# Kernel tuning notes

Hardware: AMD Instinct MI355X
Metric: run time of the kernel (lower is better)

## Reference

```python
import jax, jax.numpy as jnp
import numpy as np
from itertools import combinations_with_replacement

B, T, F, L, POLY_ORDER = 16, 2048, 128, 16, 3


def _hilbert_filter(N):
    # Matches pytorch_hilbert: H[0]=0, H[1:N//2]=2, H[N//2]=0 (even N)
    h = np.zeros(N, dtype=np.float32)
    if N % 2 == 0:
        h[1:N // 2] = 2.0
    else:
        h[1:(N + 1) // 2] = 2.0
    return jnp.asarray(h)


def hilbert(sig, axis=1):
    N = sig.shape[axis]
    Xf = jnp.fft.fft(sig, axis=axis)
    shape = [1] * sig.ndim
    shape[axis] = N
    return jnp.fft.ifft(Xf * _hilbert_filter(N).reshape(shape), axis=axis)


def _combo_indices(latent, poly_order):
    # static index arrays, grouped by degree n
    return [np.array(list(combinations_with_replacement(range(latent), n)), dtype=np.int32)
            for n in range(1, poly_order + 1)]


def compute_library(z, poly_order):
    # z: [B, T, L] -> theta: [B, T, library_dim]
    feats = []
    for combos in _combo_indices(z.shape[-1], poly_order):
        zc = z[..., combos]            # [B, T, ncomb, n]
        feats.append(jnp.prod(zc, axis=-1))  # [B, T, ncomb]
    analytic = hilbert(z, axis=1)
    feats.append(z)
    feats.append(jnp.abs(analytic))    # extract_real_component
    feats.append(jnp.angle(analytic))  # extract_imaginary_component
    return jnp.concatenate(feats, axis=-1)


def setup_inputs() -> dict:
    key = jax.random.key(0)
    ks = jax.random.split(key, 7)
    lib_dim = L + 2 * L + sum(len(c) for c in _combo_indices(L, POLY_ORDER))
    s_enc = 1.0 / np.sqrt(F)
    s_dec = 1.0 / np.sqrt(L)
    s_sin = 1.0 / np.sqrt(lib_dim)
    return {
        "x": jax.random.normal(ks[0], (B, T, F), dtype=jnp.float32),
        "W_enc": jax.random.uniform(ks[1], (L, F), jnp.float32, -s_enc, s_enc),
        "b_enc": jax.random.uniform(ks[2], (L,), jnp.float32, -s_enc, s_enc),
        "W_dec": jax.random.uniform(ks[3], (F, L), jnp.float32, -s_dec, s_dec),
        "b_dec": jax.random.uniform(ks[4], (F,), jnp.float32, -s_dec, s_dec),
        "W_sindy": jax.random.uniform(ks[5], (L, lib_dim), jnp.float32, -s_sin, s_sin),
        "b_sindy": jax.random.uniform(ks[6], (L,), jnp.float32, -s_sin, s_sin),
    }


def reference(x, W_enc, b_enc, W_dec, b_dec, W_sindy, b_sindy):
    z = jnp.einsum('btf,lf->btl', x, W_enc) + b_enc          # encoder
    theta = compute_library(z, POLY_ORDER)                    # [B,T,lib_dim]
    y_hat = jnp.einsum('btd,ld->btl', theta, W_sindy) + b_sindy
    x_hat = jnp.einsum('btl,fl->btf', z, W_dec) + b_dec       # decoder
    # Jacobian of the linear encoder w.r.t. x is the constant weight matrix
    # broadcast per (b, t): identical math to the O((B*T)^2) autograd version.
    jac_z_x = jnp.broadcast_to(W_enc, (x.shape[0], x.shape[1], L, F))
    return (y_hat, x_hat, z, jac_z_x, W_sindy, W_dec)
```

## Files before the change

### kernel.cpp

```cpp
#include <hip/hip_runtime.h>
#include <math.h>

typedef unsigned short u16;
typedef unsigned int   u32;
typedef __attribute__((ext_vector_type(4))) float f32x4;

#define OFF_ZWS   0
#define OFF_AT    524288
#define OFF_PT    1048576
#define OFF_WT    1572864
#define OFF_ZT    1589120
#define OFF_TWC   2113408
#define OFF_TWS   2115456
#define OFF_PART  2117504

#define HEAD_F4   1577952
#define R1_LO     1577952
#define R1_HI     6577952
#define R2_LO     6577952
#define R2_HI     11577952
#define R3_LO     11577952
#define R3_HI     16777216

__device__ __forceinline__ void jac_range(const float* __restrict__ Wenc,
                                          float* __restrict__ out_jac,
                                          int lo, int hi, int idx, int nth)
{
    const float* wsrc = Wenc + (size_t)((lo + idx) & 511) * 4;
    f32x4 w;
    w.x = wsrc[0]; w.y = wsrc[1]; w.z = wsrc[2]; w.w = wsrc[3];
    f32x4* j4 = (f32x4*)out_jac;
    for (int i = lo + idx; i < hi; i += nth)
        __builtin_nontemporal_store(w, j4 + i);
}

__global__ __launch_bounds__(256) void k1_encdec(
    const float* __restrict__ x, const float* __restrict__ Wenc, const float* __restrict__ benc,
    const float* __restrict__ Wdec, const float* __restrict__ bdec,
    const float* __restrict__ Wsin,
    float* __restrict__ out_z, float* __restrict__ out_xhat,
    float* __restrict__ out_Ws, float* __restrict__ out_Wd,
    float* __restrict__ z_ws, float* __restrict__ z_t, float* __restrict__ wt,
    double* __restrict__ twc_g, double* __restrict__ tws_g,
    float* __restrict__ out_jac)
{
    int tid = threadIdx.x;
    int blk = blockIdx.x;

    if (blk >= 2116) {
        jac_range(Wenc, out_jac, R1_LO, R1_HI, (blk - 2116) * 256 + tid, 262144);
        return;
    }
    if (blk >= 2048) {
        int t0 = (blk - 2048) * 256 + tid;
        if (t0 < 16256) {
            float v = Wsin[t0];
            out_Ws[t0] = v;
            int l = t0 / 1016;
            int d = t0 - l * 1016;
            wt[d * 16 + l] = v;
        } else if (t0 < 17280) {
            int k = t0 - 16256;
            double ang = -6.283185307179586476925286766559 * (double)k / 2048.0;
            double s_, c_;
            sincos(ang, &s_, &c_);
            twc_g[k] = c_;
            tws_g[k] = s_;
        }
        if (t0 < 2048) out_Wd[t0] = Wdec[t0];
        return;
    }

    __shared__ float xs[16][128];
    __shared__ float we[16][132];
    __shared__ float wd[128][17];
    __shared__ float zs[16][16];

    {
        const float4* xv = (const float4*)x + (size_t)blk * 512;
        float* dst = &xs[0][0];
        float4 a = xv[tid], b = xv[tid + 256];
        dst[tid*4+0]=a.x; dst[tid*4+1]=a.y; dst[tid*4+2]=a.z; dst[tid*4+3]=a.w;
        dst[(tid+256)*4+0]=b.x; dst[(tid+256)*4+1]=b.y; dst[(tid+256)*4+2]=b.z; dst[(tid+256)*4+3]=b.w;
    }
    {
        const float4* wev = (const float4*)Wenc;
        #pragma unroll
        for (int h = 0; h < 2; ++h) {
            int vi = tid + h * 256;
            float4 v = wev[vi];
            int base = vi * 4, row = base >> 7, col = base & 127;
            we[row][col+0]=v.x; we[row][col+1]=v.y; we[row][col+2]=v.z; we[row][col+3]=v.w;
        }
    }
    {
        const float4* wdv = (const float4*)Wdec;
        #pragma unroll
        for (int h = 0; h < 2; ++h) {
            int vi = tid + h * 256;
            float4 v = wdv[vi];
            int base = vi * 4, row = base >> 4, col = base & 15;
            wd[row][col+0]=v.x; wd[row][col+1]=v.y; wd[row][col+2]=v.z; wd[row][col+3]=v.w;
        }
    }
    __syncthreads();

    {
        int r = tid >> 4, l = tid & 15;
        float s = 0.f;
        #pragma unroll 8
        for (int f = 0; f < 128; ++f) s += xs[r][f] * we[l][f];
        float zv = s + benc[l];
        zs[r][l] = zv;
        int zo = blk * 256 + tid;
        z_ws[zo]  = zv;
        out_z[zo] = zv;
    }
    __syncthreads();

    {
        int l2 = tid >> 4, r2 = tid & 15;
        z_t[l2 * 32768 + blk * 16 + r2] = zs[r2][l2];
    }

    #pragma unroll
    for (int u = 0; u < 8; ++u) {
        int idx = u * 256 + tid;
        int rr = idx >> 7, f = idx & 127;
        float acc = bdec[f];
        #pragma unroll
        for (int ll = 0; ll < 16; ++ll) acc += zs[rr][ll] * wd[f][ll];
        out_xhat[(size_t)blk * 2048 + idx] = acc;
    }
}

__global__ __launch_bounds__(1024) void k2_hilbert(
    const float* __restrict__ z_t, const double* __restrict__ twc_g,
    const double* __restrict__ tws_g, const float* __restrict__ Wenc,
    float* __restrict__ a_t, float* __restrict__ p_t,
    float* __restrict__ out_jac)
{
    __shared__ double2 c[2048];
    __shared__ double2 tw[1024];

    int tid = threadIdx.x;
    if (blockIdx.x >= 256) {
        jac_range(Wenc, out_jac, R2_LO, R2_HI, (blockIdx.x - 256) * 1024 + tid, 524288);
        return;
    }
    int b = blockIdx.x >> 4, l = blockIdx.x & 15;
    const size_t base = (size_t)l * 32768 + (size_t)b * 2048;
    const float* zp = z_t + base;

    {
        double2 t; t.x = twc_g[tid]; t.y = tws_g[tid];
        tw[tid] = t;
    }
    {
        double2 v0; v0.x = (double)zp[tid];        v0.y = 0.0;
        double2 v1; v1.x = (double)zp[tid + 1024]; v1.y = 0.0;
        c[tid] = v0;
        c[tid + 1024] = v1;
    }
    __syncthreads();

    for (int half = 1024; half >= 1; half >>= 1) {
        int step = 1024 / half;
        int j = tid & (half - 1);
        int pos = ((tid - j) << 1) + j;
        double2 u = c[pos], v = c[pos + half];
        double2 w = tw[j * step];
        double2 s, dsc;
        s.x = u.x + v.x;  s.y = u.y + v.y;
        double br = u.x - v.x, bi = u.y - v.y;
        dsc.x = br * w.x - bi * w.y;
        dsc.y = br * w.y + bi * w.x;
        c[pos] = s;
        c[pos + half] = dsc;
        __syncthreads();
    }

    #pragma unroll
    for (int h = 0; h < 2; ++h) {
        int t = tid + h * 1024;
        double sc = (t == 0 || (t & 1)) ? 0.0 : (2.0 / 2048.0);
        double2 v = c[t];
        v.x *= sc; v.y *= sc;
        c[t] = v;
    }
    __syncthreads();

    for (int half = 1; half <= 1024; half <<= 1) {
        int step = 1024 / half;
        int j = tid & (half - 1);
        int pos = ((tid - j) << 1) + j;
        double2 u = c[pos], v = c[pos + half];
        double2 w = tw[j * step];
        double tr = v.x * w.x + v.y * w.y;
        double ti = v.y * w.x - v.x * w.y;
        double2 p0, p1;
        p0.x = u.x + tr; p0.y = u.y + ti;
        p1.x = u.x - tr; p1.y = u.y - ti;
        c[pos] = p0;
        c[pos + half] = p1;
        __syncthreads();
    }

    #pragma unroll
    for (int h = 0; h < 2; ++h) {
        int t = tid + h * 1024;
        double2 v = c[t];
        a_t[base + t] = (float)sqrt(v.x * v.x + v.y * v.y);
        p_t[base + t] = (float)atan2(v.y, v.x);
    }
}

#define EMIT2(EXPR) do {                                                    \
    if ((unsigned)(d - LO) < 127u) {                                        \
        float vv[2];                                                        \
        _Pragma("unroll") for (int p = 0; p < 2; ++p) vv[p] = (EXPR);       \
        int bb = (d - LO) << 4;                                             \
        _Pragma("unroll") for (int l = 0; l < 16; ++l) {                    \
            float w = lw[bb + l];                                           \
            acc[0][l] = fmaf(vv[0], w, acc[0][l]);                          \
            acc[1][l] = fmaf(vv[1], w, acc[1][l]);                          \
        }                                                                   \
    }                                                                       \
    ++d;                                                                    \
} while (0)

__global__ __launch_bounds__(256, 2) void k3_yhat(
    const float* __restrict__ z_ws, const float* __restrict__ a_t,
    const float* __restrict__ p_t, const float* __restrict__ wt,
    const float* __restrict__ Wenc,
    float* __restrict__ part, float* __restrict__ out_jac)
{
    __shared__ float lw[2032];
    int tid = threadIdx.x;
    if (blockIdx.x >= 512) {
        jac_range(Wenc, out_jac, R3_LO, R3_HI, (blockIdx.x - 512) * 256 + tid, 262144);
        return;
    }
    int slice = blockIdx.x >> 6;
    int ptgrp = blockIdx.x & 63;
    int LO = slice * 127;
    int base = ptgrp * 512;

    {
        const float4* src = (const float4*)(wt + LO * 16);
        float4* dst = (float4*)lw;
        for (int i = tid; i < 508; i += 256) dst[i] = src[i];
    }
    __syncthreads();

    float z[2][16], av[2][16], pv[2][16], acc[2][16];
    #pragma unroll
    for (int p = 0; p < 2; ++p) {
        int bt = base + p * 256 + tid;
        const float4* zp = (const float4*)(z_ws + (size_t)bt * 16);
        #pragma unroll
        for (int q = 0; q < 4; ++q) {
            float4 v = zp[q];
            z[p][q*4+0]=v.x; z[p][q*4+1]=v.y; z[p][q*4+2]=v.z; z[p][q*4+3]=v.w;
        }
    }
    if (LO >= 880) {
        #pragma unroll
        for (int p = 0; p < 2; ++p) {
            int bt = base + p * 256 + tid;
            #pragma unroll
            for (int l = 0; l < 16; ++l) {
                av[p][l] = a_t[(size_t)l * 32768 + bt];
                pv[p][l] = p_t[(size_t)l * 32768 + bt];
            }
        }
    } else {
        #pragma unroll
        for (int p = 0; p < 2; ++p)
            #pragma unroll
            for (int l = 0; l < 16; ++l) { av[p][l] = 0.f; pv[p][l] = 0.f; }
    }
    #pragma unroll
    for (int p = 0; p < 2; ++p)
        #pragma unroll
        for (int l = 0; l < 16; ++l) acc[p][l] = 0.f;

    int d = 0;
    #pragma unroll
    for (int i = 0; i < 16; ++i) EMIT2(z[p][i]);
    #pragma unroll
    for (int i = 0; i < 16; ++i)
        #pragma unroll
        for (int j = i; j < 16; ++j) EMIT2(z[p][i] * z[p][j]);
    #pragma unroll
    for (int i = 0; i < 16; ++i)
        #pragma unroll
        for (int j = i; j < 16; ++j)
            #pragma unroll
            for (int k = j; k < 16; ++k) EMIT2(z[p][i] * z[p][j] * z[p][k]);
    #pragma unroll
    for (int i = 0; i < 16; ++i) EMIT2(z[p][i]);
    #pragma unroll
    for (int i = 0; i < 16; ++i) EMIT2(av[p][i]);
    #pragma unroll
    for (int i = 0; i < 16; ++i) EMIT2(pv[p][i]);

    #pragma unroll
    for (int p = 0; p < 2; ++p) {
        int bt = base + p * 256 + tid;
        float4* pp = (float4*)(part + (size_t)slice * 524288 + (size_t)bt * 16);
        #pragma unroll
        for (int q = 0; q < 4; ++q) {
            float4 v;
            v.x = acc[p][q*4+0]; v.y = acc[p][q*4+1];
            v.z = acc[p][q*4+2]; v.w = acc[p][q*4+3];
            pp[q] = v;
        }
    }
}

__global__ __launch_bounds__(256) void k3_reduce(
    const float* __restrict__ part, const float* __restrict__ bsin,
    float* __restrict__ out_y)
{
    int i0 = blockIdx.x * 256 + threadIdx.x;
    float4 s = ((const float4*)bsin)[i0 & 3];
    const float4* p4 = (const float4*)part;
    #pragma unroll
    for (int sl = 0; sl < 8; ++sl) {
        float4 v = p4[(size_t)sl * 131072 + i0];
        s.x += v.x; s.y += v.y; s.z += v.z; s.w += v.w;
    }
    ((float4*)out_y)[i0] = s;
}

__global__ __launch_bounds__(256) void k4_jac_head(
    const float* __restrict__ Wenc, float* __restrict__ out_jac)
{
    jac_range(Wenc, out_jac, 0, HEAD_F4, blockIdx.x * 256 + threadIdx.x, 393216);
}

extern "C" void kernel_launch(void* const* d_in, const int* in_sizes, int n_in,
                              void* d_out, int out_size, void* d_ws, size_t ws_size,
                              hipStream_t stream)
{
    const float* x  = (const float*)d_in[0];
    const float* We = (const float*)d_in[1];
    const float* be = (const float*)d_in[2];
    const float* Wd = (const float*)d_in[3];
    const float* bd = (const float*)d_in[4];
    const float* Ws = (const float*)d_in[5];
    const float* bs = (const float*)d_in[6];

    float* out  = (float*)d_out;
    float* o_y  = out;
    float* o_xh = out + 524288;
    float* o_z  = out + 4718592;
    float* o_j  = out + 5242880;
    float* o_Ws = out + 72351744;
    float* o_Wd = out + 72368000;

    float*  z_ws  = o_j + OFF_ZWS;
    float*  a_t   = o_j + OFF_AT;
    float*  p_t   = o_j + OFF_PT;
    float*  wt    = o_j + OFF_WT;
    float*  z_t   = o_j + OFF_ZT;
    double* twc_g = (double*)(o_j + OFF_TWC);
    double* tws_g = (double*)(o_j + OFF_TWS);
    float*  part  = o_j + OFF_PART;

    hipLaunchKernelGGL(k1_encdec, dim3(3140), dim3(256), 0, stream,
                       x, We, be, Wd, bd, Ws, o_z, o_xh, o_Ws, o_Wd,
                       z_ws, z_t, wt, twc_g, tws_g, o_j);
    hipLaunchKernelGGL(k2_hilbert, dim3(768), dim3(1024), 0, stream,
                       z_t, twc_g, tws_g, We, a_t, p_t, o_j);
    hipLaunchKernelGGL(k3_yhat, dim3(1536), dim3(256), 0, stream,
                       z_ws, a_t, p_t, wt, We, part, o_j);
    hipLaunchKernelGGL(k3_reduce, dim3(512), dim3(256), 0, stream,
                       part, bs, o_y);
    hipLaunchKernelGGL(k4_jac_head, dim3(1536), dim3(256), 0, stream,
                       We, o_j);
}
```

Before: 388.6 us.

## Fold duplicate z weights, move Hilbert terms to tail, shorten FFT syncs

Adds the weights of the duplicated linear z features into the first-degree weights, so the second z block is dropped from the library GEMM. The main y_hat kernel now covers only the 968 polynomial features: 8 slices of 121 features, 4 points per thread, and a 256-block grid. The abs/angle Hilbert features are folded into a new tail kernel that also does the slice reduction and bias. In the Hilbert FFT, the inner butterfly stages with half of 64 or less use __threadfence_block instead of __syncthreads, and the even/odd filter is applied by zeroing odd bins directly. This cuts redundant FMAs and barriers, but the higher register pressure without the occupancy hint and the fence-only stages carry a risk if data crosses wave boundaries.

```diff
diff --git a/kernel.cpp b/kernel.cpp
--- a/kernel.cpp
+++ b/kernel.cpp
@@ -58,6 +58,7 @@
             out_Ws[t0] = v;
             int l = t0 / 1016;
             int d = t0 - l * 1016;
+            if (d < 16) v += Wsin[t0 + 968];
             wt[d * 16 + l] = v;
         } else if (t0 < 17280) {
             int k = t0 - 16256;
@@ -164,7 +165,7 @@
     }
     __syncthreads();
 
-    for (int half = 1024; half >= 1; half >>= 1) {
+    for (int half = 1024; half >= 128; half >>= 1) {
         int step = 1024 / half;
         int j = tid & (half - 1);
         int pos = ((tid - j) << 1) + j;
@@ -179,18 +180,50 @@
         c[pos + half] = dsc;
         __syncthreads();
     }
-
-    #pragma unroll
-    for (int h = 0; h < 2; ++h) {
-        int t = tid + h * 1024;
-        double sc = (t == 0 || (t & 1)) ? 0.0 : (2.0 / 2048.0);
-        double2 v = c[t];
-        v.x *= sc; v.y *= sc;
-        c[t] = v;
-    }
-    __syncthreads();
-
-    for (int half = 1; half <= 1024; half <<= 1) {
+    for (int half = 64; half >= 1; half >>= 1) {
+        int step = 1024 / half;
+        int j = tid & (half - 1);
+        int pos = ((tid - j) << 1) + j;
+        double2 u = c[pos], v = c[pos + half];
+        double2 w = tw[j * step];
+        double2 s, dsc;
+        s.x = u.x + v.x;  s.y = u.y + v.y;
+        double br = u.x - v.x, bi = u.y - v.y;
+        dsc.x = br * w.x - bi * w.y;
+        dsc.y = br * w.y + bi * w.x;
+        c[pos] = s;
+        c[pos + half] = dsc;
+        __threadfence_block();
+    }
+
+    {
+        int p0 = tid << 1;
+        double sc0 = (p0 == 0) ? 0.0 : (2.0 / 2048.0);
+        double2 v0 = c[p0];
+        v0.x *= sc0; v0.y *= sc0;
+        c[p0] = v0;
+        double2 zz; zz.x = 0.0; zz.y = 0.0;
+        c[p0 + 1] = zz;
+        __threadfence_block();
+    }
+
+    for (int half = 1; half <= 64; half <<= 1) {
+        int step = 1024 / half;
+        int j = tid & (half - 1);
+        int pos = ((tid - j) << 1) + j;
+        double2 u = c[pos], v = c[pos + half];
+        double2 w = tw[j * step];
+        double tr = v.x * w.x + v.y * w.y;
+        double ti = v.y * w.x - v.x * w.y;
+        double2 p0, p1;
+        p0.x = u.x + tr; p0.y = u.y + ti;
+        p1.x = u.x - tr; p1.y = u.y - ti;
+        c[pos] = p0;
+        c[pos + half] = p1;
+        __threadfence_block();
+    }
+    __syncthreads();
+    for (int half = 128; half <= 1024; half <<= 1) {
         int step = 1024 / half;
         int j = tid & (half - 1);
         int pos = ((tid - j) << 1) + j;
@@ -215,47 +248,46 @@
     }
 }
 
-#define EMIT2(EXPR) do {                                                    \
-    if ((unsigned)(d - LO) < 127u) {                                        \
-        float vv[2];                                                        \
-        _Pragma("unroll") for (int p = 0; p < 2; ++p) vv[p] = (EXPR);       \
+#define EMIT4(EXPR) do {                                                    \
+    if ((unsigned)(d - LO) < 121u) {                                        \
+        float vv[4];                                                        \
+        _Pragma("unroll") for (int p = 0; p < 4; ++p) vv[p] = (EXPR);       \
         int bb = (d - LO) << 4;                                             \
         _Pragma("unroll") for (int l = 0; l < 16; ++l) {                    \
             float w = lw[bb + l];                                           \
-            acc[0][l] = fmaf(vv[0], w, acc[0][l]);                          \
-            acc[1][l] = fmaf(vv[1], w, acc[1][l]);                          \
+            _Pragma("unroll") for (int p = 0; p < 4; ++p)                   \
+                acc[p][l] = fmaf(vv[p], w, acc[p][l]);                      \
         }                                                                   \
     }                                                                       \
     ++d;                                                                    \
 } while (0)
 
-__global__ __launch_bounds__(256, 2) void k3_yhat(
-    const float* __restrict__ z_ws, const float* __restrict__ a_t,
-    const float* __restrict__ p_t, const float* __restrict__ wt,
+__global__ __launch_bounds__(256) void k3_yhat(
+    const float* __restrict__ z_ws, const float* __restrict__ wt,
     const float* __restrict__ Wenc,
     float* __restrict__ part, float* __restrict__ out_jac)
 {
-    __shared__ float lw[2032];
+    __shared__ float lw[1936];
     int tid = threadIdx.x;
-    if (blockIdx.x >= 512) {
-        jac_range(Wenc, out_jac, R3_LO, R3_HI, (blockIdx.x - 512) * 256 + tid, 262144);
+    if (blockIdx.x >= 256) {
+        jac_range(Wenc, out_jac, R3_LO, R3_HI, (blockIdx.x - 256) * 256 + tid, 262144);
         return;
     }
-    int slice = blockIdx.x >> 6;
-    int ptgrp = blockIdx.x & 63;
-    int LO = slice * 127;
-    int base = ptgrp * 512;
+    int slice = blockIdx.x >> 5;
+    int ptgrp = blockIdx.x & 31;
+    int LO = slice * 121;
+    int base = ptgrp * 1024;
 
     {
         const float4* src = (const float4*)(wt + LO * 16);
         float4* dst = (float4*)lw;
-        for (int i = tid; i < 508; i += 256) dst[i] = src[i];
-    }
-    __syncthreads();
-
-    float z[2][16], av[2][16], pv[2][16], acc[2][16];
-    #pragma unroll
-    for (int p = 0; p < 2; ++p) {
+        for (int i = tid; i < 484; i += 256) dst[i] = src[i];
+    }
+    __syncthreads();
+
+    float z[4][16], acc[4][16];
+    #pragma unroll
+    for (int p = 0; p < 4; ++p) {
         int bt = base + p * 256 + tid;
         const float4* zp = (const float4*)(z_ws + (size_t)bt * 16);
         #pragma unroll
@@ -264,49 +296,27 @@
             z[p][q*4+0]=v.x; z[p][q*4+1]=v.y; z[p][q*4+2]=v.z; z[p][q*4+3]=v.w;
         }
     }
-    if (LO >= 880) {
-        #pragma unroll
-        for (int p = 0; p < 2; ++p) {
-            int bt = base + p * 256 + tid;
-            #pragma unroll
-            for (int l = 0; l < 16; ++l) {
-                av[p][l] = a_t[(size_t)l * 32768 + bt];
-                pv[p][l] = p_t[(size_t)l * 32768 + bt];
-            }
-        }
-    } else {
-        #pragma unroll
-        for (int p = 0; p < 2; ++p)
-            #pragma unroll
-            for (int l = 0; l < 16; ++l) { av[p][l] = 0.f; pv[p][l] = 0.f; }
-    }
-    #pragma unroll
-    for (int p = 0; p < 2; ++p)
+    #pragma unroll
+    for (int p = 0; p < 4; ++p)
         #pragma unroll
         for (int l = 0; l < 16; ++l) acc[p][l] = 0.f;
 
     int d = 0;
     #pragma unroll
-    for (int i = 0; i < 16; ++i) EMIT2(z[p][i]);
+    for (int i = 0; i < 16; ++i) EMIT4(z[p][i]);
     #pragma unroll
     for (int i = 0; i < 16; ++i)
         #pragma unroll
-        for (int j = i; j < 16; ++j) EMIT2(z[p][i] * z[p][j]);
+        for (int j = i; j < 16; ++j) EMIT4(z[p][i] * z[p][j]);
     #pragma unroll
     for (int i = 0; i < 16; ++i)
         #pragma unroll
         for (int j = i; j < 16; ++j)
             #pragma unroll
-            for (int k = j; k < 16; ++k) EMIT2(z[p][i] * z[p][j] * z[p][k]);
-    #pragma unroll
-    for (int i = 0; i < 16; ++i) EMIT2(z[p][i]);
-    #pragma unroll
-    for (int i = 0; i < 16; ++i) EMIT2(av[p][i]);
-    #pragma unroll
-    for (int i = 0; i < 16; ++i) EMIT2(pv[p][i]);
-
-    #pragma unroll
-    for (int p = 0; p < 2; ++p) {
+            for (int k = j; k < 16; ++k) EMIT4(z[p][i] * z[p][j] * z[p][k]);
+
+    #pragma unroll
+    for (int p = 0; p < 4; ++p) {
         int bt = base + p * 256 + tid;
         float4* pp = (float4*)(part + (size_t)slice * 524288 + (size_t)bt * 16);
         #pragma unroll
@@ -319,19 +329,57 @@
     }
 }
 
-__global__ __launch_bounds__(256) void k3_reduce(
-    const float* __restrict__ part, const float* __restrict__ bsin,
-    float* __restrict__ out_y)
-{
-    int i0 = blockIdx.x * 256 + threadIdx.x;
-    float4 s = ((const float4*)bsin)[i0 & 3];
-    const float4* p4 = (const float4*)part;
+__global__ __launch_bounds__(256) void k3_tail(
+    const float* __restrict__ part, const float* __restrict__ a_t,
+    const float* __restrict__ p_t, const float* __restrict__ wt,
+    const float* __restrict__ bsin, float* __restrict__ out_y)
+{
+    __shared__ float lw[512];
+    int tid = threadIdx.x;
+    if (tid < 128) {
+        ((float4*)lw)[tid] = ((const float4*)(wt + 984 * 16))[tid];
+    }
+    __syncthreads();
+
+    int bt = blockIdx.x * 256 + tid;
+    float acc[16];
+    {
+        const float4* bp = (const float4*)bsin;
+        #pragma unroll
+        for (int q = 0; q < 4; ++q) {
+            float4 v = bp[q];
+            acc[q*4+0]=v.x; acc[q*4+1]=v.y; acc[q*4+2]=v.z; acc[q*4+3]=v.w;
+        }
+    }
     #pragma unroll
     for (int sl = 0; sl < 8; ++sl) {
-        float4 v = p4[(size_t)sl * 131072 + i0];
-        s.x += v.x; s.y += v.y; s.z += v.z; s.w += v.w;
-    }
-    ((float4*)out_y)[i0] = s;
+        const float4* pp = (const float4*)(part + (size_t)sl * 524288 + (size_t)bt * 16);
+        #pragma unroll
+        for (int q = 0; q < 4; ++q) {
+            float4 v = pp[q];
+            acc[q*4+0]+=v.x; acc[q*4+1]+=v.y; acc[q*4+2]+=v.z; acc[q*4+3]+=v.w;
+        }
+    }
+    #pragma unroll
+    for (int i = 0; i < 16; ++i) {
+        float av = a_t[(size_t)i * 32768 + bt];
+        #pragma unroll
+        for (int l = 0; l < 16; ++l) acc[l] = fmaf(av, lw[i * 16 + l], acc[l]);
+    }
+    #pragma unroll
+    for (int i = 0; i < 16; ++i) {
+        float pv = p_t[(size_t)i * 32768 + bt];
+        #pragma unroll
+        for (int l = 0; l < 16; ++l) acc[l] = fmaf(pv, lw[256 + i * 16 + l], acc[l]);
+    }
+
+    float4* yp = (float4*)(out_y + (size_t)bt * 16);
+    #pragma unroll
+    for (int q = 0; q < 4; ++q) {
+        float4 v;
+        v.x = acc[q*4+0]; v.y = acc[q*4+1]; v.z = acc[q*4+2]; v.w = acc[q*4+3];
+        yp[q] = v;
+    }
 }
 
 __global__ __launch_bounds__(256) void k4_jac_head(
@@ -374,10 +422,10 @@
                        z_ws, z_t, wt, twc_g, tws_g, o_j);
     hipLaunchKernelGGL(k2_hilbert, dim3(768), dim3(1024), 0, stream,
                        z_t, twc_g, tws_g, We, a_t, p_t, o_j);
-    hipLaunchKernelGGL(k3_yhat, dim3(1536), dim3(256), 0, stream,
-                       z_ws, a_t, p_t, wt, We, part, o_j);
-    hipLaunchKernelGGL(k3_reduce, dim3(512), dim3(256), 0, stream,
-                       part, bs, o_y);
+    hipLaunchKernelGGL(k3_yhat, dim3(1280), dim3(256), 0, stream,
+                       z_ws, wt, We, part, o_j);
+    hipLaunchKernelGGL(k3_tail, dim3(128), dim3(256), 0, stream,
+                       part, a_t, p_t, wt, bs, o_y);
     hipLaunchKernelGGL(k4_jac_head, dim3(1536), dim3(256), 0, stream,
                        We, o_j);
 }
```

Result: slower. 420.7 us (+8.3%).

## Fold duplicate z weights into linear terms and move Hilbert features to reduce kernel

Applied to the files above, without the earlier changes.

The library contains z twice, so the transposed SINDy weights for the duplicate z columns are added into the degree-1 weights, removing 16 library terms. The amplitude and phase contributions are moved out of the slice-parallel yhat kernel into the reduction kernel, which now also computes the 32-term matvec per point. This lets the slices cover only the polynomial terms with less divergence and fewer registers. The cost is that the tail kernel runs only 128 blocks, does more work per thread and reads part with a strided per-thread pattern.

```diff
diff --git a/kernel.cpp b/kernel.cpp
--- a/kernel.cpp
+++ b/kernel.cpp
@@ -58,6 +58,7 @@
             out_Ws[t0] = v;
             int l = t0 / 1016;
             int d = t0 - l * 1016;
+            if (d < 16) v += Wsin[t0 + 968];
             wt[d * 16 + l] = v;
         } else if (t0 < 17280) {
             int k = t0 - 16256;
@@ -216,7 +217,7 @@
 }
 
 #define EMIT2(EXPR) do {                                                    \
-    if ((unsigned)(d - LO) < 127u) {                                        \
+    if ((unsigned)(d - LO) < 121u) {                                        \
         float vv[2];                                                        \
         _Pragma("unroll") for (int p = 0; p < 2; ++p) vv[p] = (EXPR);       \
         int bb = (d - LO) << 4;                                             \
@@ -230,12 +231,11 @@
 } while (0)
 
 __global__ __launch_bounds__(256, 2) void k3_yhat(
-    const float* __restrict__ z_ws, const float* __restrict__ a_t,
-    const float* __restrict__ p_t, const float* __restrict__ wt,
+    const float* __restrict__ z_ws, const float* __restrict__ wt,
     const float* __restrict__ Wenc,
     float* __restrict__ part, float* __restrict__ out_jac)
 {
-    __shared__ float lw[2032];
+    __shared__ float lw[1936];
     int tid = threadIdx.x;
     if (blockIdx.x >= 512) {
         jac_range(Wenc, out_jac, R3_LO, R3_HI, (blockIdx.x - 512) * 256 + tid, 262144);
@@ -243,17 +243,17 @@
     }
     int slice = blockIdx.x >> 6;
     int ptgrp = blockIdx.x & 63;
-    int LO = slice * 127;
+    int LO = slice * 121;
     int base = ptgrp * 512;
 
     {
         const float4* src = (const float4*)(wt + LO * 16);
         float4* dst = (float4*)lw;
-        for (int i = tid; i < 508; i += 256) dst[i] = src[i];
-    }
-    __syncthreads();
-
-    float z[2][16], av[2][16], pv[2][16], acc[2][16];
+        for (int i = tid; i < 484; i += 256) dst[i] = src[i];
+    }
+    __syncthreads();
+
+    float z[2][16], acc[2][16];
     #pragma unroll
     for (int p = 0; p < 2; ++p) {
         int bt = base + p * 256 + tid;
@@ -264,22 +264,6 @@
             z[p][q*4+0]=v.x; z[p][q*4+1]=v.y; z[p][q*4+2]=v.z; z[p][q*4+3]=v.w;
         }
     }
-    if (LO >= 880) {
-        #pragma unroll
-        for (int p = 0; p < 2; ++p) {
-            int bt = base + p * 256 + tid;
-            #pragma unroll
-            for (int l = 0; l < 16; ++l) {
-                av[p][l] = a_t[(size_t)l * 32768 + bt];
-                pv[p][l] = p_t[(size_t)l * 32768 + bt];
-            }
-        }
-    } else {
-        #pragma unroll
-        for (int p = 0; p < 2; ++p)
-            #pragma unroll
-            for (int l = 0; l < 16; ++l) { av[p][l] = 0.f; pv[p][l] = 0.f; }
-    }
     #pragma unroll
     for (int p = 0; p < 2; ++p)
         #pragma unroll
@@ -298,12 +282,6 @@
         for (int j = i; j < 16; ++j)
             #pragma unroll
             for (int k = j; k < 16; ++k) EMIT2(z[p][i] * z[p][j] * z[p][k]);
-    #pragma unroll
-    for (int i = 0; i < 16; ++i) EMIT2(z[p][i]);
-    #pragma unroll
-    for (int i = 0; i < 16; ++i) EMIT2(av[p][i]);
-    #pragma unroll
-    for (int i = 0; i < 16; ++i) EMIT2(pv[p][i]);
 
     #pragma unroll
     for (int p = 0; p < 2; ++p) {
@@ -319,19 +297,57 @@
     }
 }
 
-__global__ __launch_bounds__(256) void k3_reduce(
-    const float* __restrict__ part, const float* __restrict__ bsin,
-    float* __restrict__ out_y)
-{
-    int i0 = blockIdx.x * 256 + threadIdx.x;
-    float4 s = ((const float4*)bsin)[i0 & 3];
-    const float4* p4 = (const float4*)part;
+__global__ __launch_bounds__(256) void k3_tail(
+    const float* __restrict__ part, const float* __restrict__ a_t,
+    const float* __restrict__ p_t, const float* __restrict__ wt,
+    const float* __restrict__ bsin, float* __restrict__ out_y)
+{
+    __shared__ float lw[512];
+    int tid = threadIdx.x;
+    if (tid < 128) {
+        ((float4*)lw)[tid] = ((const float4*)(wt + 984 * 16))[tid];
+    }
+    __syncthreads();
+
+    int bt = blockIdx.x * 256 + tid;
+    float acc[16];
+    {
+        const float4* bp = (const float4*)bsin;
+        #pragma unroll
+        for (int q = 0; q < 4; ++q) {
+            float4 v = bp[q];
+            acc[q*4+0]=v.x; acc[q*4+1]=v.y; acc[q*4+2]=v.z; acc[q*4+3]=v.w;
+        }
+    }
     #pragma unroll
     for (int sl = 0; sl < 8; ++sl) {
-        float4 v = p4[(size_t)sl * 131072 + i0];
-        s.x += v.x; s.y += v.y; s.z += v.z; s.w += v.w;
-    }
-    ((float4*)out_y)[i0] = s;
+        const float4* pp = (const float4*)(part + (size_t)sl * 524288 + (size_t)bt * 16);
+        #pragma unroll
+        for (int q = 0; q < 4; ++q) {
+            float4 v = pp[q];
+            acc[q*4+0]+=v.x; acc[q*4+1]+=v.y; acc[q*4+2]+=v.z; acc[q*4+3]+=v.w;
+        }
+    }
+    #pragma unroll
+    for (int i = 0; i < 16; ++i) {
+        float av = a_t[(size_t)i * 32768 + bt];
+        #pragma unroll
+        for (int l = 0; l < 16; ++l) acc[l] = fmaf(av, lw[i * 16 + l], acc[l]);
+    }
+    #pragma unroll
+    for (int i = 0; i < 16; ++i) {
+        float pv = p_t[(size_t)i * 32768 + bt];
+        #pragma unroll
+        for (int l = 0; l < 16; ++l) acc[l] = fmaf(pv, lw[256 + i * 16 + l], acc[l]);
+    }
+
+    float4* yp = (float4*)(out_y + (size_t)bt * 16);
+    #pragma unroll
+    for (int q = 0; q < 4; ++q) {
+        float4 v;
+        v.x = acc[q*4+0]; v.y = acc[q*4+1]; v.z = acc[q*4+2]; v.w = acc[q*4+3];
+        yp[q] = v;
+    }
 }
 
 __global__ __launch_bounds__(256) void k4_jac_head(
@@ -375,9 +391,9 @@
     hipLaunchKernelGGL(k2_hilbert, dim3(768), dim3(1024), 0, stream,
                        z_t, twc_g, tws_g, We, a_t, p_t, o_j);
     hipLaunchKernelGGL(k3_yhat, dim3(1536), dim3(256), 0, stream,
-                       z_ws, a_t, p_t, wt, We, part, o_j);
-    hipLaunchKernelGGL(k3_reduce, dim3(512), dim3(256), 0, stream,
-                       part, bs, o_y);
+                       z_ws, wt, We, part, o_j);
+    hipLaunchKernelGGL(k3_tail, dim3(128), dim3(256), 0, stream,
+                       part, a_t, p_t, wt, bs, o_y);
     hipLaunchKernelGGL(k4_jac_head, dim3(1536), dim3(256), 0, stream,
                        We, o_j);
 }
```

After: 380.5 us. -2.1%, faster.
